# Kernel tuning notes

Measured on AMD Instinct MI355X. Metric: run time of the kernel, lower is better.

Reference implementation:

```python
import jax, jax.numpy as jnp
import numpy as np

DIM = 256
NH = 8
WS = 4  # window size (min(4, .) = 4 for all three scales)


def _rel_pos_index(ws):
    # Swin relative position index, static numpy constant
    coords = np.stack(np.meshgrid(np.arange(ws), np.arange(ws), indexing='ij')).reshape(2, -1)
    rc = (coords[:, :, None] - coords[:, None, :]).transpose(1, 2, 0).copy()
    rc[:, :, 0] += ws - 1
    rc[:, :, 1] += ws - 1
    rc[:, :, 0] *= 2 * ws - 1
    return rc.sum(-1)  # (ws*ws, ws*ws)


def _layernorm(x, g, b):
    m = x.mean(-1, keepdims=True)
    v = x.var(-1, keepdims=True)
    return (x - m) / jnp.sqrt(v + 1e-5) * g + b


def _conv1x1(x, w, b):
    # x: (B, Cin, H, W), w: (Cout, Cin)
    return jnp.einsum('bchw,oc->bohw', x, w) + b[None, :, None, None]


def _up(x, th, tw):
    # bilinear, half-pixel centers == torch align_corners=False
    B, C, _, _ = x.shape
    return jax.image.resize(x, (B, C, th, tw), 'bilinear')


def _down(x):
    B, C, H, W = x.shape
    return x.reshape(B, C, H // 2, 2, W // 2, 2).mean(axis=(3, 5))


def _wmha(x, H, W, qkv_w, qkv_b, proj_w, proj_b, rpb):
    # x: (B, H*W, C) windowed multi-head attention with relative position bias
    B, N, C = x.shape
    hd = C // NH
    scale = hd ** -0.5
    xs = x.reshape(B, H, W, C)
    pr = (-W) % WS
    pb = (-H) % WS
    if pr or pb:
        xs = jnp.pad(xs, ((0, 0), (0, pb), (0, pr), (0, 0)))
    Hp, Wp = H + pb, W + pr
    nwh, nww = Hp // WS, Wp // WS
    nt = WS * WS  # tokens per window
    # window partition -> (B*nW, nt, C)
    xw = xs.reshape(B, nwh, WS, nww, WS, C).transpose(0, 1, 3, 2, 4, 5).reshape(-1, nt, C)
    qkv = (xw @ qkv_w.T + qkv_b).reshape(-1, nt, 3, NH, hd).transpose(2, 0, 3, 1, 4)
    q, k, v = qkv[0] * scale, qkv[1], qkv[2]  # each (B*nW, NH, nt, hd)
    attn = jnp.einsum('whnd,whmd->whnm', q, k)
    rpi = _rel_pos_index(WS)
    bias = rpb[rpi.reshape(-1)].reshape(nt, nt, NH).transpose(2, 0, 1)  # (NH, nt, nt)
    attn = jax.nn.softmax(attn + bias[None], axis=-1)
    out = jnp.einsum('whnm,whmd->whnd', attn, v).transpose(0, 2, 1, 3).reshape(-1, nt, C)
    out = out @ proj_w.T + proj_b
    # window reverse
    out = out.reshape(B, nwh, nww, WS, WS, C).transpose(0, 1, 3, 2, 4, 5).reshape(B, Hp, Wp, C)
    out = out[:, :H, :W, :].reshape(B, H * W, C)
    return out


def setup_inputs() -> dict:
    key = jax.random.key(0)
    ks = jax.random.split(key, 20)
    d = DIM
    B, h1, w1, h2, w2, h3, w3 = 32, 64, 64, 32, 32, 16, 16
    N = h1 * w1 + h2 * w2 + h3 * w3
    inp = {}
    inp['x'] = jax.random.normal(ks[0], (B, N, d), jnp.float32)
    inp['norm1_g'] = jnp.ones((d,), jnp.float32)
    inp['norm1_b'] = jnp.zeros((d,), jnp.float32)
    for i, nm in enumerate(['conv1', 'conv2', 'conv3']):
        inp[nm + '_w'] = jax.random.normal(ks[1 + i], (d, 3 * d), jnp.float32) / np.sqrt(3 * d)
        inp[nm + '_b'] = jnp.zeros((d,), jnp.float32)
    for i, nm in enumerate(['mha1', 'mha2', 'mha3']):
        k0, k1, k2 = jax.random.split(ks[4 + i], 3)
        inp[nm + '_qkv_w'] = jax.random.normal(k0, (3 * d, d), jnp.float32) / np.sqrt(d)
        inp[nm + '_qkv_b'] = jnp.zeros((3 * d,), jnp.float32)
        inp[nm + '_proj_w'] = jax.random.normal(k1, (d, d), jnp.float32) / np.sqrt(d)
        inp[nm + '_proj_b'] = jnp.zeros((d,), jnp.float32)
        inp[nm + '_rpb'] = jax.random.normal(k2, ((2 * WS - 1) ** 2, NH), jnp.float32) * 0.02
    inp['norm3_g'] = jnp.ones((d,), jnp.float32)
    inp['norm3_b'] = jnp.zeros((d,), jnp.float32)
    inp['ffn_w'] = jax.random.normal(ks[8], (d, d), jnp.float32) * 0.02
    inp['ffn_b'] = jnp.zeros((d,), jnp.float32)
    inp['h1'], inp['w1'], inp['h2'], inp['w2'], inp['h3'], inp['w3'] = h1, w1, h2, w2, h3, w3
    return inp


def reference(x, norm1_g, norm1_b, conv1_w, conv1_b, conv2_w, conv2_b, conv3_w, conv3_b,
              mha1_qkv_w, mha1_qkv_b, mha1_proj_w, mha1_proj_b, mha1_rpb,
              mha2_qkv_w, mha2_qkv_b, mha2_proj_w, mha2_proj_b, mha2_rpb,
              mha3_qkv_w, mha3_qkv_b, mha3_proj_w, mha3_proj_b, mha3_rpb,
              norm3_g, norm3_b, ffn_w, ffn_b, h1, w1, h2, w2, h3, w3):
    B, N, C = x.shape
    shortcut = x
    xn = _layernorm(x, norm1_g, norm1_b)
    n1, n2 = h1 * w1, h2 * w2
    A1 = jnp.swapaxes(xn[:, :n1], 1, 2).reshape(B, C, h1, w1)
    A2 = jnp.swapaxes(xn[:, n1:n1 + n2], 1, 2).reshape(B, C, h2, w2)
    A3 = jnp.swapaxes(xn[:, n1 + n2:], 1, 2).reshape(B, C, h3, w3)
    # scale 1 fusion
    A2u = _up(A2, h1, w1)
    A3u = _up(_up(A3, h2, w2), h1, w1)
    A1f = _conv1x1(jnp.concatenate([A1, A2u, A3u], axis=1), conv1_w, conv1_b)
    # scale 2 fusion
    A2f = _conv1x1(jnp.concatenate([_down(A1), A2, _up(A3, h2, w2)], axis=1), conv2_w, conv2_b)
    # scale 3 fusion
    A3f = _conv1x1(jnp.concatenate([_down(_down(A1)), _down(A2), A3], axis=1), conv3_w, conv3_b)
    s1 = A1f.reshape(B, C, h1 * w1).swapaxes(1, 2)
    s2 = A2f.reshape(B, C, h2 * w2).swapaxes(1, 2)
    s3 = A3f.reshape(B, C, h3 * w3).swapaxes(1, 2)
    o1 = _wmha(s1, h1, w1, mha1_qkv_w, mha1_qkv_b, mha1_proj_w, mha1_proj_b, mha1_rpb)
    o2 = _wmha(s2, h2, w2, mha2_qkv_w, mha2_qkv_b, mha2_proj_w, mha2_proj_b, mha2_rpb)
    o3 = _wmha(s3, h3, w3, mha3_qkv_w, mha3_qkv_b, mha3_proj_w, mha3_proj_b, mha3_rpb)
    out = shortcut + jnp.concatenate([o1, o2, o3], axis=1)
    out = out + (_layernorm(out, norm3_g, norm3_b) @ ffn_w.T + ffn_b)
    return out
```

## Files before the change

### kernel.cpp

```cpp
#include <hip/hip_runtime.h>


typedef unsigned short ushort_t;
typedef unsigned int   uint32;
typedef __attribute__((ext_vector_type(8))) short short8;
typedef __attribute__((ext_vector_type(4))) float f32x4;

#define GLOBAL_AS __attribute__((address_space(1)))
#define LDS_AS    __attribute__((address_space(3)))

__device__ __forceinline__ float b2f(ushort_t h) {
    union { uint32 u; float f; } x; x.u = ((uint32)h) << 16; return x.f;
}
__device__ __forceinline__ ushort_t f2b(float f) {
    union { float f; uint32 u; } x; x.f = f;
    uint32 u = x.u;
    return (ushort_t)((u + 0x7FFFu + ((u >> 16) & 1u)) >> 16);
}
__device__ __forceinline__ void async_ld16(const void* g, void* l) {
    __builtin_amdgcn_global_load_lds((const GLOBAL_AS uint32*)g, (LDS_AS uint32*)l, 16, 0, 0);
}

template<bool SPLIT>
__global__ __launch_bounds__(256)
void ln_kernel(const float* __restrict__ x, const float* __restrict__ g,
               const float* __restrict__ bb,
               ushort_t* d0, ushort_t* d1, ushort_t* d2, int ntok)
{
    int wid  = blockIdx.x * 4 + (threadIdx.x >> 6);
    int lane = threadIdx.x & 63;
    if (wid >= ntok) return;
    const float* row = x + (size_t)wid * 256;
    float4 v = *(const float4*)(row + lane * 4);
    float s  = v.x + v.y + v.z + v.w;
    float s2 = v.x*v.x + v.y*v.y + v.z*v.z + v.w*v.w;
#pragma unroll
    for (int mask = 1; mask < 64; mask <<= 1) {
        s  += __shfl_xor(s,  mask);
        s2 += __shfl_xor(s2, mask);
    }
    float mean = s * (1.f/256.f);
    float var  = s2 * (1.f/256.f) - mean*mean;
    float rstd = rsqrtf(var + 1e-5f);
    ushort_t* dst;
    if (SPLIT) {
        int b = wid / 5376, n = wid % 5376;
        if      (n < 4096) dst = d0 + ((size_t)b*4096 + n)        * 256;
        else if (n < 5120) dst = d1 + ((size_t)b*1024 + (n-4096)) * 256;
        else               dst = d2 + ((size_t)b*256  + (n-5120)) * 256;
    } else {
        dst = d0 + (size_t)wid * 256;
    }
    int c = lane * 4;
    float4 gg = *(const float4*)(g  + c);
    float4 bv = *(const float4*)(bb + c);
    ushort4 o;
    o.x = f2b((v.x-mean)*rstd*gg.x + bv.x);
    o.y = f2b((v.y-mean)*rstd*gg.y + bv.y);
    o.z = f2b((v.z-mean)*rstd*gg.z + bv.z);
    o.w = f2b((v.w-mean)*rstd*gg.w + bv.w);
    *(ushort4*)(dst + c) = o;
}

__global__ __launch_bounds__(256)
void repack(const float* c1, const float* c2, const float* c3,
            const float* q1, const float* q2, const float* q3,
            const float* p1, const float* p2, const float* p3,
            const float* fw,
            ushort_t* Wf, ushort_t* Wq, ushort_t* Wp, ushort_t* Wff)
{
    int idx = blockIdx.x * 256 + threadIdx.x;
    if (idx < 3*768*256) {
        int j = idx / (768*256), rem = idx % (768*256);
        int o = rem >> 8, c = rem & 255;
        const float* src = (o < 256) ? c1 : (o < 512 ? c2 : c3);
        Wf[idx] = f2b(src[(size_t)(o & 255)*768 + j*256 + c]);
        return;
    }
    int i2 = idx - 3*768*256;
    if (i2 < 3*768*256) {
        const float* src = (i2 < 196608) ? q1 : (i2 < 393216 ? q2 : q3);
        Wq[i2] = f2b(src[i2 % 196608]);
        return;
    }
    int i3 = i2 - 3*768*256;
    if (i3 < 3*65536) {
        const float* src = (i3 < 65536) ? p1 : (i3 < 131072 ? p2 : p3);
        Wp[i3] = f2b(src[i3 % 65536]);
        return;
    }
    int i4 = i3 - 3*65536;
    if (i4 < 65536) Wff[i4] = f2b(fw[i4]);
}

template<int MODE, bool HAS_BIAS>
__global__ __launch_bounds__(256)
void gemm_k256(const ushort_t* __restrict__ A, const ushort_t* __restrict__ Bw,
               const float* __restrict__ bias, const float* __restrict__ resid,
               void* __restrict__ outp, int M, int Nout,
               int n_per_b, int N_total, int off)
{
    __shared__ ushort_t As[128][64];
    __shared__ ushort_t Bs[128][64];
    const int K = 256;
    int lane = threadIdx.x & 63;
    int w    = threadIdx.x >> 6;
    int m0 = blockIdx.y * 128;
    int n0 = blockIdx.x * 128;
    int wm = w >> 1, wn = w & 1;

    f32x4 acc[4][4];
#pragma unroll
    for (int m = 0; m < 4; ++m)
#pragma unroll
        for (int n = 0; n < 4; ++n) acc[m][n] = f32x4{0.f,0.f,0.f,0.f};

    int sr = lane >> 3;
    int sc = (lane & 7) * 8;

    for (int k0 = 0; k0 < K; k0 += 64) {
        __syncthreads();
#pragma unroll
        for (int q = 0; q < 4; ++q) {
            int rr = (w*4 + q) * 8;
            const ushort_t* ga = A  + (size_t)(m0 + rr + sr) * K + (k0 + sc);
            const ushort_t* gb = Bw + (size_t)(n0 + rr + sr) * K + (k0 + sc);
            async_ld16(ga, &As[rr][0]);
            async_ld16(gb, &Bs[rr][0]);
        }
        __syncthreads();
        int row = lane & 15;
        int kof = 8 * (lane >> 4);
#pragma unroll
        for (int kk = 0; kk < 64; kk += 32) {
            short8 af[4], bf[4];
#pragma unroll
            for (int m = 0; m < 4; ++m)
                af[m] = *(const short8*)&As[wm*64 + m*16 + row][kk + kof];
#pragma unroll
            for (int n = 0; n < 4; ++n)
                bf[n] = *(const short8*)&Bs[wn*64 + n*16 + row][kk + kof];
#pragma unroll
            for (int m = 0; m < 4; ++m)
#pragma unroll
                for (int n = 0; n < 4; ++n)
                    acc[m][n] = __builtin_amdgcn_mfma_f32_16x16x32_bf16(
                        af[m], bf[n], acc[m][n], 0, 0, 0);
        }
    }

    int cr = (lane >> 4) * 4;
    int cc = lane & 15;
#pragma unroll
    for (int m = 0; m < 4; ++m) {
#pragma unroll
        for (int r = 0; r < 4; ++r) {
            int grow = m0 + wm*64 + m*16 + cr + r;
            size_t orow;
            if (MODE == 1) {
                int bidx = grow / n_per_b;
                int t    = grow - bidx * n_per_b;
                orow = (size_t)bidx * N_total + off + t;
            } else {
                orow = (size_t)grow;
            }
#pragma unroll
            for (int n = 0; n < 4; ++n) {
                int col = n0 + wn*64 + n*16 + cc;
                float v = acc[m][n][r];
                if (HAS_BIAS) v += bias[col];
                if (MODE == 0) {
                    ((ushort_t*)outp)[(size_t)grow * Nout + col] = f2b(v);
                } else if (MODE == 1) {
                    float* o = (float*)outp;
                    v += resid[orow * 256 + col];
                    o[orow * 256 + col] = v;
                } else {
                    float* o = (float*)outp;
                    o[orow * 256 + col] += v;
                }
            }
        }
    }
}

__device__ __forceinline__ void up_taps(int i, int S, int& j0, int& j1,
                                        float& w0, float& w1)
{
    int t = i >> 1;
    if (i & 1) { j0 = t; j1 = (t+1 < S) ? t+1 : S-1; w0 = 0.75f; w1 = 0.25f; }
    else       { j0 = (t > 0) ? t-1 : 0; j1 = t;     w0 = 0.25f; w1 = 0.75f; }
}

__global__ __launch_bounds__(256)
void fuse1(const ushort_t* __restrict__ Q1, const ushort_t* __restrict__ Q2,
           const ushort_t* __restrict__ Q3, const float* __restrict__ bias,
           ushort_t* __restrict__ s1o)
{
    int c = threadIdx.x;
    int p = blockIdx.x;
    int b = p >> 12, pix = p & 4095;
    int y = pix >> 6, x = pix & 63;
    float acc = b2f(Q1[(size_t)p * 768 + c]);
    int y0,y1,x0,x1; float wy0,wy1,wx0,wx1;
    up_taps(y, 32, y0, y1, wy0, wy1);
    up_taps(x, 32, x0, x1, wx0, wx1);
    size_t q2b = (size_t)b * 1024;
    acc += wy0*wx0 * b2f(Q2[(q2b + y0*32 + x0)*768 + c]);
    acc += wy0*wx1 * b2f(Q2[(q2b + y0*32 + x1)*768 + c]);
    acc += wy1*wx0 * b2f(Q2[(q2b + y1*32 + x0)*768 + c]);
    acc += wy1*wx1 * b2f(Q2[(q2b + y1*32 + x1)*768 + c]);
    size_t q3b = (size_t)b * 256;
#pragma unroll
    for (int ay = 0; ay < 2; ++ay) {
        int   my  = ay ? y1 : y0;
        float wmy = ay ? wy1 : wy0;
        int sy0, sy1; float wsy0, wsy1;
        up_taps(my, 16, sy0, sy1, wsy0, wsy1);
#pragma unroll
        for (int ax = 0; ax < 2; ++ax) {
            int   mx  = ax ? x1 : x0;
            float wmx = ax ? wx1 : wx0;
            int sx0, sx1; float wsx0, wsx1;
            up_taps(mx, 16, sx0, sx1, wsx0, wsx1);
            float mid = wsy0*(wsx0*b2f(Q3[(q3b + sy0*16 + sx0)*768 + c]) +
                              wsx1*b2f(Q3[(q3b + sy0*16 + sx1)*768 + c]))
                      + wsy1*(wsx0*b2f(Q3[(q3b + sy1*16 + sx0)*768 + c]) +
                              wsx1*b2f(Q3[(q3b + sy1*16 + sx1)*768 + c]));
            acc += wmy * wmx * mid;
        }
    }
    acc += bias[c];
    s1o[(size_t)p * 256 + c] = f2b(acc);
}

__global__ __launch_bounds__(256)
void fuse2(const ushort_t* __restrict__ Q1, const ushort_t* __restrict__ Q2,
           const ushort_t* __restrict__ Q3, const float* __restrict__ bias,
           ushort_t* __restrict__ s2o)
{
    int c = threadIdx.x;
    int p = blockIdx.x;
    int b = p >> 10, pix = p & 1023;
    int y = pix >> 5, x = pix & 31;
    float acc = b2f(Q2[(size_t)p * 768 + 256 + c]);
    size_t q1b = (size_t)b * 4096;
    float d = 0.f;
#pragma unroll
    for (int dy = 0; dy < 2; ++dy)
#pragma unroll
        for (int dx = 0; dx < 2; ++dx)
            d += b2f(Q1[(q1b + (size_t)(2*y+dy)*64 + (2*x+dx))*768 + 256 + c]);
    acc += 0.25f * d;
    int y0,y1,x0,x1; float wy0,wy1,wx0,wx1;
    up_taps(y, 16, y0, y1, wy0, wy1);
    up_taps(x, 16, x0, x1, wx0, wx1);
    size_t q3b = (size_t)b * 256;
    acc += wy0*wx0 * b2f(Q3[(q3b + y0*16 + x0)*768 + 256 + c]);
    acc += wy0*wx1 * b2f(Q3[(q3b + y0*16 + x1)*768 + 256 + c]);
    acc += wy1*wx0 * b2f(Q3[(q3b + y1*16 + x0)*768 + 256 + c]);
    acc += wy1*wx1 * b2f(Q3[(q3b + y1*16 + x1)*768 + 256 + c]);
    acc += bias[c];
    s2o[(size_t)p * 256 + c] = f2b(acc);
}

__global__ __launch_bounds__(256)
void fuse3(const ushort_t* __restrict__ Q1, const ushort_t* __restrict__ Q2,
           const ushort_t* __restrict__ Q3, const float* __restrict__ bias,
           ushort_t* __restrict__ s3o)
{
    int c = threadIdx.x;
    int p = blockIdx.x;
    int b = p >> 8, pix = p & 255;
    int y = pix >> 4, x = pix & 15;
    float acc = b2f(Q3[(size_t)p * 768 + 512 + c]);
    size_t q1b = (size_t)b * 4096;
    float d = 0.f;
#pragma unroll
    for (int dy = 0; dy < 4; ++dy)
#pragma unroll
        for (int dx = 0; dx < 4; ++dx)
            d += b2f(Q1[(q1b + (size_t)(4*y+dy)*64 + (4*x+dx))*768 + 512 + c]);
    acc += d * 0.0625f;
    size_t q2b = (size_t)b * 1024;
    float e = 0.f;
#pragma unroll
    for (int dy = 0; dy < 2; ++dy)
#pragma unroll
        for (int dx = 0; dx < 2; ++dx)
            e += b2f(Q2[(q2b + (size_t)(2*y+dy)*32 + (2*x+dx))*768 + 512 + c]);
    acc += 0.25f * e;
    acc += bias[c];
    s3o[(size_t)p * 256 + c] = f2b(acc);
}

__global__ __launch_bounds__(256)
void attn_kernel(const ushort_t* __restrict__ qkv, ushort_t* __restrict__ outp,
                 const float* __restrict__ rpb, int Wpix, int nwx, int nw,
                 int npix, int totwaves)
{
    int gw   = (blockIdx.x * 256 + threadIdx.x) >> 6;
    int lane = threadIdx.x & 63;
    if (gw >= totwaves) return;
    int h   = gw & 7;
    int win = (gw >> 3) % nw;
    int b   = gw / (nw * 8);
    int wy = win / nwx, wx = win % nwx;
    int i = lane & 15, g = lane >> 4;
    size_t rowbase = (size_t)b * npix;
    int py = wy * 4, px = wx * 4;

    size_t rowi = (rowbase + (size_t)(py + (i >> 2)) * Wpix + px + (i & 3)) * 768;
    int koff = h * 32 + 8 * g;
    short8 kf = *(const short8*)(qkv + rowi + 256 + koff);
    short8 qf = *(const short8*)(qkv + rowi + koff);
    f32x4 stv = {0.f, 0.f, 0.f, 0.f};
    stv = __builtin_amdgcn_mfma_f32_16x16x32_bf16(kf, qf, stv, 0, 0, 0);

    const float scale = 0.17677669529663687f;
    float sv[4], p[4];
    float m = -1e30f;
#pragma unroll
    for (int r = 0; r < 4; ++r) {
        int j  = 4 * g + r;
        int dy = (i >> 2) - (j >> 2) + 3;
        int dx = (i & 3)  - (j & 3)  + 3;
        sv[r] = stv[r] * scale + rpb[(dy * 7 + dx) * 8 + h];
        m = fmaxf(m, sv[r]);
    }
    m = fmaxf(m, __shfl_xor(m, 16));
    m = fmaxf(m, __shfl_xor(m, 32));
    float sum = 0.f;
#pragma unroll
    for (int r = 0; r < 4; ++r) { p[r] = __expf(sv[r] - m); sum += p[r]; }
    sum += __shfl_xor(sum, 16);
    sum += __shfl_xor(sum, 32);
    float inv = 1.f / sum;
    unsigned pa = (unsigned)f2b(p[0]*inv) | ((unsigned)f2b(p[1]*inv) << 16);
    unsigned pb = (unsigned)f2b(p[2]*inv) | ((unsigned)f2b(p[3]*inv) << 16);

    int srcA = (i + 32 * g) & 63;
    int srcB = (i + 32 * g + 16) & 63;
    unsigned a0 = (unsigned)__shfl((int)pa, srcA);
    unsigned a1 = (unsigned)__shfl((int)pb, srcA);
    unsigned b0 = (unsigned)__shfl((int)pa, srcB);
    unsigned b1 = (unsigned)__shfl((int)pb, srcB);
    if (g >= 2) { a0 = a1 = b0 = b1 = 0; }
    union { unsigned u[4]; short8 v; } pf;
    pf.u[0] = a0; pf.u[1] = a1; pf.u[2] = b0; pf.u[3] = b1;

    size_t orow = (rowbase + (size_t)(py + (i >> 2)) * Wpix + px + (i & 3)) * 256;
#pragma unroll
    for (int h2 = 0; h2 < 2; ++h2) {
        union { ushort_t us[8]; short8 v; } vt;
#pragma unroll
        for (int jj = 0; jj < 8; ++jj) vt.us[jj] = 0;
        if (g < 2) {
#pragma unroll
            for (int jj = 0; jj < 8; ++jj) {
                int t = 8 * g + jj;
                size_t rv = (rowbase + (size_t)(py + (t >> 2)) * Wpix + px + (t & 3)) * 768;
                vt.us[jj] = qkv[rv + 512 + h * 32 + h2 * 16 + i];
            }
        }
        f32x4 ov = {0.f, 0.f, 0.f, 0.f};
        ov = __builtin_amdgcn_mfma_f32_16x16x32_bf16(vt.v, pf.v, ov, 0, 0, 0);
        ushort4 st;
        st.x = f2b(ov[0]); st.y = f2b(ov[1]); st.z = f2b(ov[2]); st.w = f2b(ov[3]);
        *(ushort4*)(outp + orow + h * 32 + h2 * 16 + 4 * g) = st;
    }
}

extern "C" void kernel_launch(void* const* d_in, const int* in_sizes, int n_in,
                              void* d_out, int out_size, void* d_ws, size_t ws_size,
                              hipStream_t stream)
{
    (void)in_sizes; (void)n_in; (void)out_size; (void)ws_size;
    const float* x    = (const float*)d_in[0];
    const float* n1g  = (const float*)d_in[1];
    const float* n1b  = (const float*)d_in[2];
    const float* c1w  = (const float*)d_in[3];
    const float* c1b  = (const float*)d_in[4];
    const float* c2w  = (const float*)d_in[5];
    const float* c2b  = (const float*)d_in[6];
    const float* c3w  = (const float*)d_in[7];
    const float* c3b  = (const float*)d_in[8];
    const float* q1w  = (const float*)d_in[9];
    const float* q1b  = (const float*)d_in[10];
    const float* p1w  = (const float*)d_in[11];
    const float* p1b  = (const float*)d_in[12];
    const float* rpb1 = (const float*)d_in[13];
    const float* q2w  = (const float*)d_in[14];
    const float* q2b  = (const float*)d_in[15];
    const float* p2w  = (const float*)d_in[16];
    const float* p2b  = (const float*)d_in[17];
    const float* rpb2 = (const float*)d_in[18];
    const float* q3w  = (const float*)d_in[19];
    const float* q3b  = (const float*)d_in[20];
    const float* p3w  = (const float*)d_in[21];
    const float* p3b  = (const float*)d_in[22];
    const float* rpb3 = (const float*)d_in[23];
    const float* n3g  = (const float*)d_in[24];
    const float* n3b  = (const float*)d_in[25];
    const float* ffw  = (const float*)d_in[26];
    const float* ffb  = (const float*)d_in[27];
    float* out = (float*)d_out;

    const int M1 = 32 * 4096, M2 = 32 * 1024, M3 = 32 * 256;
    const int MT = M1 + M2 + M3;

    char* ws = (char*)d_ws;
    ushort_t* xn1 = (ushort_t*)ws;
    ushort_t* xn2 = xn1 + (size_t)M1 * 256;
    ushort_t* xn3 = xn2 + (size_t)M2 * 256;
    ushort_t* at1 = xn1; ushort_t* at2 = xn2; ushort_t* at3 = xn3;
    ushort_t* Q1 = (ushort_t*)(ws + 88080384);
    ushort_t* Q2 = Q1 + (size_t)M1 * 768;
    ushort_t* Q3 = Q2 + (size_t)M2 * 768;
    ushort_t* kv1 = Q1; ushort_t* kv2 = Q2; ushort_t* kv3 = Q3;
    ushort_t* s1 = (ushort_t*)(ws + 88080384 + 264241152);
    ushort_t* s2 = s1 + (size_t)M1 * 256;
    ushort_t* s3 = s2 + (size_t)M2 * 256;
    ushort_t* ln2 = s1;
    ushort_t* Wf  = (ushort_t*)(ws + 88080384 + 264241152 + 88080384);
    ushort_t* Wq  = Wf + 3*768*256;
    ushort_t* Wp  = Wq + 3*768*256;
    ushort_t* Wff = Wp + 3*256*256;

    repack<<<5632, 256, 0, stream>>>(c1w, c2w, c3w, q1w, q2w, q3w,
                                     p1w, p2w, p3w, ffw, Wf, Wq, Wp, Wff);
    ln_kernel<true><<<MT/4, 256, 0, stream>>>(x, n1g, n1b, xn1, xn2, xn3, MT);
    gemm_k256<0,false><<<dim3(6, M1/128), 256, 0, stream>>>(xn1, Wf,          nullptr, nullptr, Q1, M1, 768, 0, 0, 0);
    gemm_k256<0,false><<<dim3(6, M2/128), 256, 0, stream>>>(xn2, Wf+196608,   nullptr, nullptr, Q2, M2, 768, 0, 0, 0);
    gemm_k256<0,false><<<dim3(6, M3/128), 256, 0, stream>>>(xn3, Wf+393216,   nullptr, nullptr, Q3, M3, 768, 0, 0, 0);
    fuse1<<<M1, 256, 0, stream>>>(Q1, Q2, Q3, c1b, s1);
    fuse2<<<M2, 256, 0, stream>>>(Q1, Q2, Q3, c2b, s2);
    fuse3<<<M3, 256, 0, stream>>>(Q1, Q2, Q3, c3b, s3);
    gemm_k256<0,true><<<dim3(6, M1/128), 256, 0, stream>>>(s1, Wq,         q1b, nullptr, kv1, M1, 768, 0, 0, 0);
    gemm_k256<0,true><<<dim3(6, M2/128), 256, 0, stream>>>(s2, Wq+196608,  q2b, nullptr, kv2, M2, 768, 0, 0, 0);
    gemm_k256<0,true><<<dim3(6, M3/128), 256, 0, stream>>>(s3, Wq+393216,  q3b, nullptr, kv3, M3, 768, 0, 0, 0);
    attn_kernel<<<16384, 256, 0, stream>>>(kv1, at1, rpb1, 64, 16, 256, 4096, 65536);
    attn_kernel<<< 4096, 256, 0, stream>>>(kv2, at2, rpb2, 32,  8,  64, 1024, 16384);
    attn_kernel<<< 1024, 256, 0, stream>>>(kv3, at3, rpb3, 16,  4,  16,  256,  4096);
    gemm_k256<1,true><<<dim3(2, M1/128), 256, 0, stream>>>(at1, Wp,        p1b, x, out, M1, 256, 4096, 5376, 0);
    gemm_k256<1,true><<<dim3(2, M2/128), 256, 0, stream>>>(at2, Wp+65536,  p2b, x, out, M2, 256, 1024, 5376, 4096);
    gemm_k256<1,true><<<dim3(2, M3/128), 256, 0, stream>>>(at3, Wp+131072, p3b, x, out, M3, 256,  256, 5376, 5120);
    ln_kernel<false><<<MT/4, 256, 0, stream>>>(out, n3g, n3b, ln2, nullptr, nullptr, MT);
    gemm_k256<2,true><<<dim3(2, MT/128), 256, 0, stream>>>(ln2, Wff, ffb, nullptr, out, MT, 256, MT, 0, 0);
}
```

Measured before the change: 1.309 ms.

## Restructure scale-fusion convs: downsample inputs first, upsample only needed partial products

```diff
diff --git a/kernel.cpp b/kernel.cpp
--- a/kernel.cpp
+++ b/kernel.cpp
@@ -46,8 +46,8 @@
     if (SPLIT) {
         int b = wid / 5376, n = wid % 5376;
         if      (n < 4096) dst = d0 + ((size_t)b*4096 + n)        * 256;
-        else if (n < 5120) dst = d1 + ((size_t)b*1024 + (n-4096)) * 256;
-        else               dst = d2 + ((size_t)b*256  + (n-5120)) * 256;
+        else if (n < 5120) dst = d1 + ((size_t)b*1024 + (n-4096)) * 512;
+        else               dst = d2 + ((size_t)b*256  + (n-5120)) * 768;
     } else {
         dst = d0 + (size_t)wid * 256;
     }
@@ -66,43 +66,82 @@
 void repack(const float* c1, const float* c2, const float* c3,
             const float* q1, const float* q2, const float* q3,
             const float* p1, const float* p2, const float* p3,
-            const float* fw,
-            ushort_t* Wf, ushort_t* Wq, ushort_t* Wp, ushort_t* Wff)
+            const float* fw, ushort_t* W)
 {
     int idx = blockIdx.x * 256 + threadIdx.x;
-    if (idx < 3*768*256) {
-        int j = idx / (768*256), rem = idx % (768*256);
-        int o = rem >> 8, c = rem & 255;
-        const float* src = (o < 256) ? c1 : (o < 512 ? c2 : c3);
-        Wf[idx] = f2b(src[(size_t)(o & 255)*768 + j*256 + c]);
-        return;
-    }
-    int i2 = idx - 3*768*256;
-    if (i2 < 3*768*256) {
-        const float* src = (i2 < 196608) ? q1 : (i2 < 393216 ? q2 : q3);
-        Wq[i2] = f2b(src[i2 % 196608]);
-        return;
-    }
-    int i3 = i2 - 3*768*256;
-    if (i3 < 3*65536) {
-        const float* src = (i3 < 65536) ? p1 : (i3 < 131072 ? p2 : p3);
-        Wp[i3] = f2b(src[i3 % 65536]);
-        return;
-    }
-    int i4 = i3 - 3*65536;
-    if (i4 < 65536) Wff[i4] = f2b(fw[i4]);
+    const float* src; int off;
+    if      (idx <  196608) { src = c1; off = idx; }
+    else if (idx <  393216) { src = c2; off = idx -  196608; }
+    else if (idx <  589824) { src = c3; off = idx -  393216; }
+    else if (idx <  786432) { src = q1; off = idx -  589824; }
+    else if (idx <  983040) { src = q2; off = idx -  786432; }
+    else if (idx < 1179648) { src = q3; off = idx -  983040; }
+    else if (idx < 1245184) { src = p1; off = idx - 1179648; }
+    else if (idx < 1310720) { src = p2; off = idx - 1245184; }
+    else if (idx < 1376256) { src = p3; off = idx - 1310720; }
+    else                    { src = fw; off = idx - 1376256; }
+    W[idx] = f2b(src[off]);
+}
+
+__global__ __launch_bounds__(256)
+void down1(const ushort_t* __restrict__ xn1, ushort_t* __restrict__ A2cat)
+{
+    int t = blockIdx.x * 256 + threadIdx.x;
+    int p = t >> 5, c0 = (t & 31) * 8;
+    int b = p >> 10, pix = p & 1023;
+    int y = pix >> 5, x = pix & 31;
+    size_t base = (size_t)b * 4096;
+    float acc[8] = {0,0,0,0,0,0,0,0};
+#pragma unroll
+    for (int dy = 0; dy < 2; ++dy)
+#pragma unroll
+    for (int dx = 0; dx < 2; ++dx) {
+        short8 v = *(const short8*)(xn1 + (base + (size_t)(2*y+dy)*64 + (2*x+dx)) * 256 + c0);
+#pragma unroll
+        for (int j = 0; j < 8; ++j) acc[j] += b2f((ushort_t)v[j]);
+    }
+    union { ushort_t us[8]; short8 v; } o;
+#pragma unroll
+    for (int j = 0; j < 8; ++j) o.us[j] = f2b(acc[j] * 0.25f);
+    *(short8*)(A2cat + (size_t)p * 512 + c0) = o.v;
+}
+
+__global__ __launch_bounds__(256)
+void down2(const ushort_t* __restrict__ A2cat, ushort_t* __restrict__ A3cat)
+{
+    int t = blockIdx.x * 256 + threadIdx.x;
+    int half = t >> 18;
+    int r = t & 262143;
+    int p = r >> 5, c0 = (r & 31) * 8;
+    int b = p >> 8, pix = p & 255;
+    int y = pix >> 4, x = pix & 15;
+    int co = half * 256;
+    size_t base = (size_t)b * 1024;
+    float acc[8] = {0,0,0,0,0,0,0,0};
+#pragma unroll
+    for (int dy = 0; dy < 2; ++dy)
+#pragma unroll
+    for (int dx = 0; dx < 2; ++dx) {
+        short8 v = *(const short8*)(A2cat + (base + (size_t)(2*y+dy)*32 + (2*x+dx)) * 512 + co + c0);
+#pragma unroll
+        for (int j = 0; j < 8; ++j) acc[j] += b2f((ushort_t)v[j]);
+    }
+    union { ushort_t us[8]; short8 v; } o;
+#pragma unroll
+    for (int j = 0; j < 8; ++j) o.us[j] = f2b(acc[j] * 0.25f);
+    *(short8*)(A3cat + (size_t)p * 768 + co + c0) = o.v;
 }
 
 template<int MODE, bool HAS_BIAS>
 __global__ __launch_bounds__(256)
-void gemm_k256(const ushort_t* __restrict__ A, const ushort_t* __restrict__ Bw,
-               const float* __restrict__ bias, const float* __restrict__ resid,
-               void* __restrict__ outp, int M, int Nout,
-               int n_per_b, int N_total, int off)
+void gemm_bt(const ushort_t* __restrict__ A, int lda,
+             const ushort_t* __restrict__ Bw, int ldb, int K,
+             const float* __restrict__ bias, const float* __restrict__ resid,
+             void* __restrict__ outp, int Nout,
+             int n_per_b, int N_total, int off)
 {
     __shared__ ushort_t As[128][64];
     __shared__ ushort_t Bs[128][64];
-    const int K = 256;
     int lane = threadIdx.x & 63;
     int w    = threadIdx.x >> 6;
     int m0 = blockIdx.y * 128;
@@ -123,8 +162,8 @@
 #pragma unroll
         for (int q = 0; q < 4; ++q) {
             int rr = (w*4 + q) * 8;
-            const ushort_t* ga = A  + (size_t)(m0 + rr + sr) * K + (k0 + sc);
-            const ushort_t* gb = Bw + (size_t)(n0 + rr + sr) * K + (k0 + sc);
+            const ushort_t* ga = A  + (size_t)(m0 + rr + sr) * lda + (k0 + sc);
+            const ushort_t* gb = Bw + (size_t)(n0 + rr + sr) * ldb + (k0 + sc);
             async_ld16(ga, &As[rr][0]);
             async_ld16(gb, &Bs[rr][0]);
         }
@@ -193,105 +232,96 @@
 }
 
 __global__ __launch_bounds__(256)
-void fuse1(const ushort_t* __restrict__ Q1, const ushort_t* __restrict__ Q2,
-           const ushort_t* __restrict__ Q3, const float* __restrict__ bias,
-           ushort_t* __restrict__ s1o)
-{
-    int c = threadIdx.x;
-    int p = blockIdx.x;
+void fuse1v(const ushort_t* __restrict__ Q11, const ushort_t* __restrict__ Q21,
+            const ushort_t* __restrict__ Q31, ushort_t* __restrict__ s1o)
+{
+    int t = threadIdx.x;
+    int p = blockIdx.x * 8 + (t >> 5);
+    int c0 = (t & 31) * 8;
     int b = p >> 12, pix = p & 4095;
     int y = pix >> 6, x = pix & 63;
-    float acc = b2f(Q1[(size_t)p * 768 + c]);
+    float acc[8];
+    {
+        short8 v = *(const short8*)(Q11 + (size_t)p * 256 + c0);
+#pragma unroll
+        for (int j = 0; j < 8; ++j) acc[j] = b2f((ushort_t)v[j]);
+    }
     int y0,y1,x0,x1; float wy0,wy1,wx0,wx1;
     up_taps(y, 32, y0, y1, wy0, wy1);
     up_taps(x, 32, x0, x1, wx0, wx1);
+    const int   ty[2] = {y0, y1}; const float wyv[2] = {wy0, wy1};
+    const int   tx[2] = {x0, x1}; const float wxv[2] = {wx0, wx1};
     size_t q2b = (size_t)b * 1024;
-    acc += wy0*wx0 * b2f(Q2[(q2b + y0*32 + x0)*768 + c]);
-    acc += wy0*wx1 * b2f(Q2[(q2b + y0*32 + x1)*768 + c]);
-    acc += wy1*wx0 * b2f(Q2[(q2b + y1*32 + x0)*768 + c]);
-    acc += wy1*wx1 * b2f(Q2[(q2b + y1*32 + x1)*768 + c]);
+#pragma unroll
+    for (int ay = 0; ay < 2; ++ay)
+#pragma unroll
+    for (int ax = 0; ax < 2; ++ax) {
+        float wgt = wyv[ay] * wxv[ax];
+        short8 v = *(const short8*)(Q21 + (q2b + (size_t)ty[ay]*32 + tx[ax]) * 256 + c0);
+#pragma unroll
+        for (int j = 0; j < 8; ++j) acc[j] += wgt * b2f((ushort_t)v[j]);
+    }
     size_t q3b = (size_t)b * 256;
 #pragma unroll
     for (int ay = 0; ay < 2; ++ay) {
-        int   my  = ay ? y1 : y0;
-        float wmy = ay ? wy1 : wy0;
         int sy0, sy1; float wsy0, wsy1;
-        up_taps(my, 16, sy0, sy1, wsy0, wsy1);
+        up_taps(ty[ay], 16, sy0, sy1, wsy0, wsy1);
+        const int sy[2] = {sy0, sy1}; const float wsy[2] = {wsy0, wsy1};
 #pragma unroll
         for (int ax = 0; ax < 2; ++ax) {
-            int   mx  = ax ? x1 : x0;
-            float wmx = ax ? wx1 : wx0;
+            float wm = wyv[ay] * wxv[ax];
             int sx0, sx1; float wsx0, wsx1;
-            up_taps(mx, 16, sx0, sx1, wsx0, wsx1);
-            float mid = wsy0*(wsx0*b2f(Q3[(q3b + sy0*16 + sx0)*768 + c]) +
-                              wsx1*b2f(Q3[(q3b + sy0*16 + sx1)*768 + c]))
-                      + wsy1*(wsx0*b2f(Q3[(q3b + sy1*16 + sx0)*768 + c]) +
-                              wsx1*b2f(Q3[(q3b + sy1*16 + sx1)*768 + c]));
-            acc += wmy * wmx * mid;
+            up_taps(tx[ax], 16, sx0, sx1, wsx0, wsx1);
+            const int sx[2] = {sx0, sx1}; const float wsx[2] = {wsx0, wsx1};
+#pragma unroll
+            for (int iy = 0; iy < 2; ++iy)
+#pragma unroll
+            for (int ix = 0; ix < 2; ++ix) {
+                float wgt = wm * wsy[iy] * wsx[ix];
+                short8 v = *(const short8*)(Q31 + (q3b + (size_t)sy[iy]*16 + sx[ix]) * 256 + c0);
+#pragma unroll
+                for (int j = 0; j < 8; ++j) acc[j] += wgt * b2f((ushort_t)v[j]);
+            }
         }
     }
-    acc += bias[c];
-    s1o[(size_t)p * 256 + c] = f2b(acc);
-}
-
-__global__ __launch_bounds__(256)
-void fuse2(const ushort_t* __restrict__ Q1, const ushort_t* __restrict__ Q2,
-           const ushort_t* __restrict__ Q3, const float* __restrict__ bias,
-           ushort_t* __restrict__ s2o)
-{
-    int c = threadIdx.x;
-    int p = blockIdx.x;
+    union { ushort_t us[8]; short8 v; } o;
+#pragma unroll
+    for (int j = 0; j < 8; ++j) o.us[j] = f2b(acc[j]);
+    *(short8*)(s1o + (size_t)p * 256 + c0) = o.v;
+}
+
+__global__ __launch_bounds__(256)
+void fuse2v(ushort_t* __restrict__ s2, const ushort_t* __restrict__ Q32)
+{
+    int t = blockIdx.x * 256 + threadIdx.x;
+    int p = t >> 5, c0 = (t & 31) * 8;
     int b = p >> 10, pix = p & 1023;
     int y = pix >> 5, x = pix & 31;
-    float acc = b2f(Q2[(size_t)p * 768 + 256 + c]);
-    size_t q1b = (size_t)b * 4096;
-    float d = 0.f;
-#pragma unroll
-    for (int dy = 0; dy < 2; ++dy)
-#pragma unroll
-        for (int dx = 0; dx < 2; ++dx)
-            d += b2f(Q1[(q1b + (size_t)(2*y+dy)*64 + (2*x+dx))*768 + 256 + c]);
-    acc += 0.25f * d;
+    float acc[8];
+    {
+        short8 v = *(const short8*)(s2 + (size_t)p * 256 + c0);
+#pragma unroll
+        for (int j = 0; j < 8; ++j) acc[j] = b2f((ushort_t)v[j]);
+    }
     int y0,y1,x0,x1; float wy0,wy1,wx0,wx1;
     up_taps(y, 16, y0, y1, wy0, wy1);
     up_taps(x, 16, x0, x1, wx0, wx1);
+    const int   ty[2] = {y0, y1}; const float wyv[2] = {wy0, wy1};
+    const int   tx[2] = {x0, x1}; const float wxv[2] = {wx0, wx1};
     size_t q3b = (size_t)b * 256;
-    acc += wy0*wx0 * b2f(Q3[(q3b + y0*16 + x0)*768 + 256 + c]);
-    acc += wy0*wx1 * b2f(Q3[(q3b + y0*16 + x1)*768 + 256 + c]);
-    acc += wy1*wx0 * b2f(Q3[(q3b + y1*16 + x0)*768 + 256 + c]);
-    acc += wy1*wx1 * b2f(Q3[(q3b + y1*16 + x1)*768 + 256 + c]);
-    acc += bias[c];
-    s2o[(size_t)p * 256 + c] = f2b(acc);
-}
-
-__global__ __launch_bounds__(256)
-void fuse3(const ushort_t* __restrict__ Q1, const ushort_t* __restrict__ Q2,
-           const ushort_t* __restrict__ Q3, const float* __restrict__ bias,
-           ushort_t* __restrict__ s3o)
-{
-    int c = threadIdx.x;
-    int p = blockIdx.x;
-    int b = p >> 8, pix = p & 255;
-    int y = pix >> 4, x = pix & 15;
-    float acc = b2f(Q3[(size_t)p * 768 + 512 + c]);
-    size_t q1b = (size_t)b * 4096;
-    float d = 0.f;
-#pragma unroll
-    for (int dy = 0; dy < 4; ++dy)
-#pragma unroll
-        for (int dx = 0; dx < 4; ++dx)
-            d += b2f(Q1[(q1b + (size_t)(4*y+dy)*64 + (4*x+dx))*768 + 512 + c]);
-    acc += d * 0.0625f;
-    size_t q2b = (size_t)b * 1024;
-    float e = 0.f;
-#pragma unroll
-    for (int dy = 0; dy < 2; ++dy)
-#pragma unroll
-        for (int dx = 0; dx < 2; ++dx)
-            e += b2f(Q2[(q2b + (size_t)(2*y+dy)*32 + (2*x+dx))*768 + 512 + c]);
-    acc += 0.25f * e;
-    acc += bias[c];
-    s3o[(size_t)p * 256 + c] = f2b(acc);
+#pragma unroll
+    for (int ay = 0; ay < 2; ++ay)
+#pragma unroll
+    for (int ax = 0; ax < 2; ++ax) {
+        float wgt = wyv[ay] * wxv[ax];
+        short8 v = *(const short8*)(Q32 + (q3b + (size_t)ty[ay]*16 + tx[ax]) * 256 + c0);
+#pragma unroll
+        for (int j = 0; j < 8; ++j) acc[j] += wgt * b2f((ushort_t)v[j]);
+    }
+    union { ushort_t us[8]; short8 v; } o;
+#pragma unroll
+    for (int j = 0; j < 8; ++j) o.us[j] = f2b(acc[j]);
+    *(short8*)(s2 + (size_t)p * 256 + c0) = o.v;
 }
 
 __global__ __launch_bounds__(256)
@@ -410,41 +440,57 @@
     const int MT = M1 + M2 + M3;
 
     char* ws = (char*)d_ws;
-    ushort_t* xn1 = (ushort_t*)ws;
-    ushort_t* xn2 = xn1 + (size_t)M1 * 256;
-    ushort_t* xn3 = xn2 + (size_t)M2 * 256;
-    ushort_t* at1 = xn1; ushort_t* at2 = xn2; ushort_t* at3 = xn3;
-    ushort_t* Q1 = (ushort_t*)(ws + 88080384);
-    ushort_t* Q2 = Q1 + (size_t)M1 * 768;
-    ushort_t* Q3 = Q2 + (size_t)M2 * 768;
-    ushort_t* kv1 = Q1; ushort_t* kv2 = Q2; ushort_t* kv3 = Q3;
-    ushort_t* s1 = (ushort_t*)(ws + 88080384 + 264241152);
-    ushort_t* s2 = s1 + (size_t)M1 * 256;
+    ushort_t* R1 = (ushort_t*)ws;
+    ushort_t* xn1   = R1;
+    ushort_t* A2cat = R1 + 33554432;
+    ushort_t* A3cat = R1 + 50331648;
+    ushort_t* Q11   = R1 + 56623104;
+    ushort_t* Q21   = R1 + 90177536;
+    ushort_t* Q31   = R1 + 98566144;
+    ushort_t* Q32   = R1 + 100663296;
+    ushort_t* kv1 = R1;
+    ushort_t* kv2 = kv1 + (size_t)M1 * 768;
+    ushort_t* kv3 = kv2 + (size_t)M2 * 768;
+    ushort_t* ln2 = R1;
+    ushort_t* R2 = (ushort_t*)(ws + 264241152);
+    ushort_t* s1 = R2;
+    ushort_t* s2 = R2 + (size_t)M1 * 256;
     ushort_t* s3 = s2 + (size_t)M2 * 256;
-    ushort_t* ln2 = s1;
-    ushort_t* Wf  = (ushort_t*)(ws + 88080384 + 264241152 + 88080384);
-    ushort_t* Wq  = Wf + 3*768*256;
-    ushort_t* Wp  = Wq + 3*768*256;
-    ushort_t* Wff = Wp + 3*256*256;
+    ushort_t* at1 = s1; ushort_t* at2 = s2; ushort_t* at3 = s3;
+    ushort_t* W   = (ushort_t*)(ws + 264241152 + 88080384);
+    ushort_t* Wc1 = W;
+    ushort_t* Wc2 = W + 196608;
+    ushort_t* Wc3 = W + 393216;
+    ushort_t* Wq1 = W + 589824;
+    ushort_t* Wq2 = W + 786432;
+    ushort_t* Wq3 = W + 983040;
+    ushort_t* Wp1 = W + 1179648;
+    ushort_t* Wp2 = W + 1245184;
+    ushort_t* Wp3 = W + 1310720;
+    ushort_t* Wff = W + 1376256;
 
     repack<<<5632, 256, 0, stream>>>(c1w, c2w, c3w, q1w, q2w, q3w,
-                                     p1w, p2w, p3w, ffw, Wf, Wq, Wp, Wff);
-    ln_kernel<true><<<MT/4, 256, 0, stream>>>(x, n1g, n1b, xn1, xn2, xn3, MT);
-    gemm_k256<0,false><<<dim3(6, M1/128), 256, 0, stream>>>(xn1, Wf,          nullptr, nullptr, Q1, M1, 768, 0, 0, 0);
-    gemm_k256<0,false><<<dim3(6, M2/128), 256, 0, stream>>>(xn2, Wf+196608,   nullptr, nullptr, Q2, M2, 768, 0, 0, 0);
-    gemm_k256<0,false><<<dim3(6, M3/128), 256, 0, stream>>>(xn3, Wf+393216,   nullptr, nullptr, Q3, M3, 768, 0, 0, 0);
-    fuse1<<<M1, 256, 0, stream>>>(Q1, Q2, Q3, c1b, s1);
-    fuse2<<<M2, 256, 0, stream>>>(Q1, Q2, Q3, c2b, s2);
-    fuse3<<<M3, 256, 0, stream>>>(Q1, Q2, Q3, c3b, s3);
-    gemm_k256<0,true><<<dim3(6, M1/128), 256, 0, stream>>>(s1, Wq,         q1b, nullptr, kv1, M1, 768, 0, 0, 0);
-    gemm_k256<0,true><<<dim3(6, M2/128), 256, 0, stream>>>(s2, Wq+196608,  q2b, nullptr, kv2, M2, 768, 0, 0, 0);
-    gemm_k256<0,true><<<dim3(6, M3/128), 256, 0, stream>>>(s3, Wq+393216,  q3b, nullptr, kv3, M3, 768, 0, 0, 0);
+                                     p1w, p2w, p3w, ffw, W);
+    ln_kernel<true><<<MT/4, 256, 0, stream>>>(x, n1g, n1b, xn1, A2cat + 256, A3cat + 512, MT);
+    down1<<<4096, 256, 0, stream>>>(xn1, A2cat);
+    down2<<<2048, 256, 0, stream>>>(A2cat, A3cat);
+    gemm_bt<0,false><<<dim3(2, 256), 256, 0, stream>>>(A2cat + 256, 512, Wc1 + 256, 768, 256, nullptr, nullptr, Q21, 256, 0, 0, 0);
+    gemm_bt<0,false><<<dim3(2,  64), 256, 0, stream>>>(A3cat + 512, 768, Wc1 + 512, 768, 256, nullptr, nullptr, Q31, 256, 0, 0, 0);
+    gemm_bt<0,false><<<dim3(2,  64), 256, 0, stream>>>(A3cat + 512, 768, Wc2 + 512, 768, 256, nullptr, nullptr, Q32, 256, 0, 0, 0);
+    gemm_bt<0,true><<<dim3(2,1024), 256, 0, stream>>>(xn1,   256, Wc1, 768, 256, c1b, nullptr, Q11, 256, 0, 0, 0);
+    gemm_bt<0,true><<<dim3(2, 256), 256, 0, stream>>>(A2cat, 512, Wc2, 768, 512, c2b, nullptr, s2,  256, 0, 0, 0);
+    gemm_bt<0,true><<<dim3(2,  64), 256, 0, stream>>>(A3cat, 768, Wc3, 768, 768, c3b, nullptr, s3,  256, 0, 0, 0);
+    fuse1v<<<16384, 256, 0, stream>>>(Q11, Q21, Q31, s1);
+    fuse2v<<< 4096, 256, 0, stream>>>(s2, Q32);
+    gemm_bt<0,true><<<dim3(6,1024), 256, 0, stream>>>(s1, 256, Wq1, 256, 256, q1b, nullptr, kv1, 768, 0, 0, 0);
+    gemm_bt<0,true><<<dim3(6, 256), 256, 0, stream>>>(s2, 256, Wq2, 256, 256, q2b, nullptr, kv2, 768, 0, 0, 0);
+    gemm_bt<0,true><<<dim3(6,  64), 256, 0, stream>>>(s3, 256, Wq3, 256, 256, q3b, nullptr, kv3, 768, 0, 0, 0);
     attn_kernel<<<16384, 256, 0, stream>>>(kv1, at1, rpb1, 64, 16, 256, 4096, 65536);
     attn_kernel<<< 4096, 256, 0, stream>>>(kv2, at2, rpb2, 32,  8,  64, 1024, 16384);
     attn_kernel<<< 1024, 256, 0, stream>>>(kv3, at3, rpb3, 16,  4,  16,  256,  4096);
-    gemm_k256<1,true><<<dim3(2, M1/128), 256, 0, stream>>>(at1, Wp,        p1b, x, out, M1, 256, 4096, 5376, 0);
-    gemm_k256<1,true><<<dim3(2, M2/128), 256, 0, stream>>>(at2, Wp+65536,  p2b, x, out, M2, 256, 1024, 5376, 4096);
-    gemm_k256<1,true><<<dim3(2, M3/128), 256, 0, stream>>>(at3, Wp+131072, p3b, x, out, M3, 256,  256, 5376, 5120);
+    gemm_bt<1,true><<<dim3(2,1024), 256, 0, stream>>>(at1, 256, Wp1, 256, 256, p1b, x, out, 256, 4096, 5376, 0);
+    gemm_bt<1,true><<<dim3(2, 256), 256, 0, stream>>>(at2, 256, Wp2, 256, 256, p2b, x, out, 256, 1024, 5376, 4096);
+    gemm_bt<1,true><<<dim3(2,  64), 256, 0, stream>>>(at3, 256, Wp3, 256, 256, p3b, x, out, 256,  256, 5376, 5120);
     ln_kernel<false><<<MT/4, 256, 0, stream>>>(out, n3g, n3b, ln2, nullptr, nullptr, MT);
-    gemm_k256<2,true><<<dim3(2, MT/128), 256, 0, stream>>>(ln2, Wff, ffb, nullptr, out, MT, 256, MT, 0, 0);
-}
+    gemm_bt<2,true><<<dim3(2, MT/128), 256, 0, stream>>>(ln2, 256, Wff, 256, 256, ffb, nullptr, out, 256, MT, 0, 0);
+}
```

Result: faster. 1.057 ms (-19.2%).
